# Performance work log

Hardware: AMD Instinct MI355X
Metric: run time of the kernel (lower is better)

Reference implementation:

```python
import jax, jax.numpy as jnp
import numpy as np

B, N, T, F = 64, 1024, 64, 8
IN = T * F      # LSTMCell input size = 512
H = T           # LSTMCell hidden size = 64


def setup_inputs() -> dict:
    key = jax.random.key(0)
    k1, k2, k3, k4, k5 = jax.random.split(key, 5)
    s_ih = 1.0 / np.sqrt(H)
    return {
        "x": jax.random.normal(k1, (B, N, T, F), dtype=jnp.float32),
        "W_ih": jax.random.uniform(k2, (4 * H, IN), minval=-s_ih, maxval=s_ih, dtype=jnp.float32),
        "W_hh": jax.random.uniform(k3, (4 * H, H), minval=-s_ih, maxval=s_ih, dtype=jnp.float32),
        "b_ih": jax.random.uniform(k4, (4 * H,), minval=-s_ih, maxval=s_ih, dtype=jnp.float32),
        "b_hh": jax.random.uniform(k5, (4 * H,), minval=-s_ih, maxval=s_ih, dtype=jnp.float32),
    }


def _lstm_scan(x_seq, W_ih, W_hh, b_ih, b_hh):
    # x_seq: (n, b, t*f). Recurrent scan over the node dimension.
    b = x_seq.shape[1]
    h0 = jnp.zeros((b, H), dtype=x_seq.dtype)
    c0 = jnp.zeros((b, H), dtype=x_seq.dtype)
    # Precompute input projections for all steps at once (big GEMM).
    xg = jnp.einsum('nbi,gi->nbg', x_seq, W_ih) + b_ih + b_hh  # (n, b, 4H)

    def step(carry, xg_t):
        h, c = carry
        gates = xg_t + h @ W_hh.T                # (b, 4H)
        i, f, g, o = jnp.split(gates, 4, axis=-1)
        i = jax.nn.sigmoid(i)
        f = jax.nn.sigmoid(f)
        g = jnp.tanh(g)
        o = jax.nn.sigmoid(o)
        c_new = f * c + i * g
        h_new = o * jnp.tanh(c_new)
        return (h_new, c_new), h_new

    _, hs = jax.lax.scan(step, (h0, c0), xg)     # hs: (n, b, H)
    return hs


def reference(x, W_ih, W_hh, b_ih, b_hh):
    b, n, t, f = x.shape
    x_em = x.reshape(b, n, t * f).transpose(1, 0, 2)   # (n, b, t*f)
    hs = _lstm_scan(x_em, W_ih, W_hh, b_ih, b_hh)      # (n, b, t)
    return hs.transpose(1, 0, 2)                        # (b, n, t)
```

## Files before the change

### kernel.cpp

```cpp
#include <hip/hip_runtime.h>
#include <math.h>

#define B_  64
#define N_  1024
#define H_  64
#define IN_ 512
#define G4  256

__global__ __launch_bounds__(256) void gemm_xg_kernel(
    const float* __restrict__ x,
    const float* __restrict__ Wih,
    const float* __restrict__ bih,
    const float* __restrict__ bhh,
    float* __restrict__ xg)
{
    __shared__ float As[32][68];
    __shared__ float Bs[32][68];

    const int tid = threadIdx.x;
    const int g0  = blockIdx.x * 64;
    const int m0  = blockIdx.y * 64;

    const int tx = tid & 15;
    const int ty = tid >> 4;

    const int arow = tid >> 3;
    const int ak4  = tid & 7;
    const int brow = tid >> 2;
    const int bk4  = tid & 3;

    float acc[4][4] = {{0.f}};

    for (int k0 = 0; k0 < IN_; k0 += 32) {
        #pragma unroll
        for (int half = 0; half < 2; ++half) {
            const int ml = arow + half * 32;
            const int m  = m0 + ml;
            const int bb = m & 63;
            const int nn = m >> 6;
            const float4 v = *(const float4*)&x[((size_t)(bb * N_ + nn)) * IN_ + k0 + ak4 * 4];
            As[ak4 * 4 + 0][ml] = v.x;
            As[ak4 * 4 + 1][ml] = v.y;
            As[ak4 * 4 + 2][ml] = v.z;
            As[ak4 * 4 + 3][ml] = v.w;
        }
        #pragma unroll
        for (int half = 0; half < 2; ++half) {
            const int kq = bk4 + half * 4;
            const float4 v = *(const float4*)&Wih[(size_t)(g0 + brow) * IN_ + k0 + kq * 4];
            Bs[kq * 4 + 0][brow] = v.x;
            Bs[kq * 4 + 1][brow] = v.y;
            Bs[kq * 4 + 2][brow] = v.z;
            Bs[kq * 4 + 3][brow] = v.w;
        }
        __syncthreads();

        #pragma unroll
        for (int k = 0; k < 32; ++k) {
            const float4 av = *(const float4*)&As[k][ty * 4];
            const float4 bv = *(const float4*)&Bs[k][tx * 4];
            const float ar[4] = {av.x, av.y, av.z, av.w};
            const float br[4] = {bv.x, bv.y, bv.z, bv.w};
            #pragma unroll
            for (int i = 0; i < 4; ++i)
                #pragma unroll
                for (int j = 0; j < 4; ++j)
                    acc[i][j] = fmaf(ar[i], br[j], acc[i][j]);
        }
        __syncthreads();
    }

    float bias[4];
    #pragma unroll
    for (int j = 0; j < 4; ++j)
        bias[j] = bih[g0 + tx * 4 + j] + bhh[g0 + tx * 4 + j];

    #pragma unroll
    for (int i = 0; i < 4; ++i) {
        const int m = m0 + ty * 4 + i;
        float4 o;
        o.x = acc[i][0] + bias[0];
        o.y = acc[i][1] + bias[1];
        o.z = acc[i][2] + bias[2];
        o.w = acc[i][3] + bias[3];
        *(float4*)&xg[(size_t)m * G4 + g0 + tx * 4] = o;
    }
}

__device__ __forceinline__ float fast_rcp(float x) {
    return __builtin_amdgcn_rcpf(x);
}

template <int CTRL>
__device__ __forceinline__ float dppf(float x) {
    return __int_as_float(__builtin_amdgcn_mov_dpp(
        __float_as_int(x), CTRL, 0xF, 0xF, true));
}
#define DPP_QSWAP1 0xB1
#define DPP_SHR4   0x114
#define DPP_SHR2   0x112

__global__ __launch_bounds__(512) void lstm_scan_kernel(
    const float* __restrict__ xg,
    const float* __restrict__ Whh,
    float* __restrict__ out)
{
    const int t    = threadIdx.x;
    const int bb   = blockIdx.x;
    const int w    = t >> 6;
    const int ln   = t & 63;
    const int half = ln & 1;
    const int gidx = (ln >> 1) & 3;
    const int cell = (w << 3) | (ln >> 3);
    const int grow = (gidx << 6) | cell;

    __shared__ float h_sh[2][64];

    float4 w4[8];
    {
        const float* wrow = &Whh[(size_t)grow * H_ + half * 32];
        #pragma unroll
        for (int q = 0; q < 8; ++q)
            w4[q] = *(const float4*)&wrow[q * 4];
    }
    #pragma unroll
    for (int q = 0; q < 8; ++q)
        asm volatile("" : "+v"(w4[q].x), "+v"(w4[q].y), "+v"(w4[q].z), "+v"(w4[q].w));

    const float Ac = (gidx == 2) ? 1.f : 0.f;
    const float Bc = (gidx == 2) ? -2.f : 1.f;
    const float Cc = (gidx == 2) ? 2.f : -1.f;
    const bool  is_o = (gidx == 3);
    const bool  is_writer = ((ln & 7) == 6);
    const bool  carries_xg = (half == 0);

    float c = 0.f;
    if (t < 64) h_sh[0][t] = 0.f;
    __syncthreads();

    int cur = 0;
    const size_t xg_base = (size_t)bb * G4 + grow;
    const size_t xg_nstride = (size_t)B_ * G4;

    float p0 = xg[xg_base + 0 * xg_nstride];
    float p1 = xg[xg_base + 1 * xg_nstride];
    float p2 = xg[xg_base + 2 * xg_nstride];
    float p3 = xg[xg_base + 3 * xg_nstride];

    auto step = [&](int n, float xg_cur) {
        const float* hb = &h_sh[cur][half * 32];
        float b0 = carries_xg ? xg_cur : 0.f;
        float b1 = 0.f, b2 = 0.f, b3 = 0.f;
        float b4 = 0.f, b5 = 0.f, b6 = 0.f, b7 = 0.f;
        #pragma unroll
        for (int q = 0; q < 8; q += 2) {
            const float4 h0 = *(const float4*)&hb[q * 4];
            const float4 h1 = *(const float4*)&hb[q * 4 + 4];
            b0 = fmaf(w4[q].x,     h0.x, b0);
            b1 = fmaf(w4[q].y,     h0.y, b1);
            b2 = fmaf(w4[q].z,     h0.z, b2);
            b3 = fmaf(w4[q].w,     h0.w, b3);
            b4 = fmaf(w4[q + 1].x, h1.x, b4);
            b5 = fmaf(w4[q + 1].y, h1.y, b5);
            b6 = fmaf(w4[q + 1].z, h1.z, b6);
            b7 = fmaf(w4[q + 1].w, h1.w, b7);
        }
        float acc = ((b0 + b4) + (b1 + b5)) + ((b2 + b6) + (b3 + b7));
        acc += dppf<DPP_QSWAP1>(acc);

        const float v = fmaf(Bc, fast_rcp(1.f + __expf(Cc * acc)), Ac);

        const float u  = is_o ? c : v;
        const float t_ = dppf<DPP_SHR4>(u);
        const float w_ = u * t_;
        const float s  = w_ + dppf<DPP_SHR2>(w_);
        const float th = fmaf(-2.f, fast_rcp(1.f + __expf(2.f * s)), 1.f);
        const float h  = v * th;
        c = s;

        if (is_writer) {
            h_sh[cur ^ 1][cell] = h;
            out[((size_t)bb * N_ + n) * H_ + cell] = h;
        }

        asm volatile("s_waitcnt lgkmcnt(0)" ::: "memory");
        __builtin_amdgcn_s_barrier();
        asm volatile("" ::: "memory");

        cur ^= 1;
    };

    for (int n = 0; n < N_; n += 4) {
        step(n + 0, p0);
        p0 = xg[xg_base + (size_t)((n + 4 < N_) ? n + 4 : N_ - 1) * xg_nstride];
        step(n + 1, p1);
        p1 = xg[xg_base + (size_t)((n + 5 < N_) ? n + 5 : N_ - 1) * xg_nstride];
        step(n + 2, p2);
        p2 = xg[xg_base + (size_t)((n + 6 < N_) ? n + 6 : N_ - 1) * xg_nstride];
        step(n + 3, p3);
        p3 = xg[xg_base + (size_t)((n + 7 < N_) ? n + 7 : N_ - 1) * xg_nstride];
    }
}

extern "C" void kernel_launch(void* const* d_in, const int* in_sizes, int n_in,
                              void* d_out, int out_size, void* d_ws, size_t ws_size,
                              hipStream_t stream)
{
    const float* x   = (const float*)d_in[0];
    const float* Wih = (const float*)d_in[1];
    const float* Whh = (const float*)d_in[2];
    const float* bih = (const float*)d_in[3];
    const float* bhh = (const float*)d_in[4];
    float* out = (float*)d_out;
    float* xg  = (float*)d_ws;

    dim3 ggrid(4, 1024);
    gemm_xg_kernel<<<ggrid, 256, 0, stream>>>(x, Wih, bih, bhh, xg);
    lstm_scan_kernel<<<64, 512, 0, stream>>>(xg, Whh, out);
}
```

Baseline: 707.5 us.

## Assign one full gate row per lane and halve scan block to four waves

The scan kernel now gives each lane a complete 64-wide W_hh row, held as 16 float4 registers in a rotated order. The four gates of a cell sit in a lane quad, and h values are rotated across the quad with DPP so each lane reads only a quarter of h from LDS. This drops the cross-lane partial-sum reduction and cuts the block from 512 to 256 threads, so each per-step barrier synchronises fewer waves. The cost is more VGPRs per lane (64 for weights) and a longer serial FMA chain per lane.

```diff
diff --git a/kernel.cpp b/kernel.cpp
--- a/kernel.cpp
+++ b/kernel.cpp
@@ -96,11 +96,20 @@
     return __int_as_float(__builtin_amdgcn_mov_dpp(
         __float_as_int(x), CTRL, 0xF, 0xF, true));
 }
-#define DPP_QSWAP1 0xB1
-#define DPP_SHR4   0x114
-#define DPP_SHR2   0x112
-
-__global__ __launch_bounds__(512) void lstm_scan_kernel(
+#define DPP_ROT1   0x39
+#define DPP_G_T    0x44
+#define DPP_G_S    0x90
+
+__device__ __forceinline__ float4 qrot1(float4 v) {
+    float4 r;
+    r.x = dppf<DPP_ROT1>(v.x);
+    r.y = dppf<DPP_ROT1>(v.y);
+    r.z = dppf<DPP_ROT1>(v.z);
+    r.w = dppf<DPP_ROT1>(v.w);
+    return r;
+}
+
+__global__ __launch_bounds__(256, 1) void lstm_scan_kernel(
     const float* __restrict__ xg,
     const float* __restrict__ Whh,
     float* __restrict__ out)
@@ -109,30 +118,29 @@
     const int bb   = blockIdx.x;
     const int w    = t >> 6;
     const int ln   = t & 63;
-    const int half = ln & 1;
-    const int gidx = (ln >> 1) & 3;
-    const int cell = (w << 3) | (ln >> 3);
-    const int grow = (gidx << 6) | cell;
+    const int qpos = ln & 3;
+    const int cell = (w << 4) | (ln >> 2);
+    const int grow = (qpos << 6) | cell;
 
     __shared__ float h_sh[2][64];
 
-    float4 w4[8];
+    float4 wst[16];
     {
-        const float* wrow = &Whh[(size_t)grow * H_ + half * 32];
-        #pragma unroll
-        for (int q = 0; q < 8; ++q)
-            w4[q] = *(const float4*)&wrow[q * 4];
+        const float* wrow = &Whh[(size_t)grow * H_];
+        #pragma unroll
+        for (int r = 0; r < 4; ++r)
+            #pragma unroll
+            for (int s = 0; s < 4; ++s)
+                wst[r * 4 + s] = *(const float4*)&wrow[(4 * r + ((qpos + s) & 3)) * 4];
     }
     #pragma unroll
-    for (int q = 0; q < 8; ++q)
-        asm volatile("" : "+v"(w4[q].x), "+v"(w4[q].y), "+v"(w4[q].z), "+v"(w4[q].w));
-
-    const float Ac = (gidx == 2) ? 1.f : 0.f;
-    const float Bc = (gidx == 2) ? -2.f : 1.f;
-    const float Cc = (gidx == 2) ? 2.f : -1.f;
-    const bool  is_o = (gidx == 3);
-    const bool  is_writer = ((ln & 7) == 6);
-    const bool  carries_xg = (half == 0);
+    for (int q = 0; q < 16; ++q)
+        asm volatile("" : "+v"(wst[q].x), "+v"(wst[q].y), "+v"(wst[q].z), "+v"(wst[q].w));
+
+    const float Ac = (qpos == 2) ? 1.f : 0.f;
+    const float Bc = (qpos == 2) ? -2.f : 1.f;
+    const float Cc = (qpos == 2) ? 2.f : -1.f;
+    const bool  is_o = (qpos == 3);
 
     float c = 0.f;
     if (t < 64) h_sh[0][t] = 0.f;
@@ -148,37 +156,76 @@
     float p3 = xg[xg_base + 3 * xg_nstride];
 
     auto step = [&](int n, float xg_cur) {
-        const float* hb = &h_sh[cur][half * 32];
-        float b0 = carries_xg ? xg_cur : 0.f;
-        float b1 = 0.f, b2 = 0.f, b3 = 0.f;
-        float b4 = 0.f, b5 = 0.f, b6 = 0.f, b7 = 0.f;
-        #pragma unroll
-        for (int q = 0; q < 8; q += 2) {
-            const float4 h0 = *(const float4*)&hb[q * 4];
-            const float4 h1 = *(const float4*)&hb[q * 4 + 4];
-            b0 = fmaf(w4[q].x,     h0.x, b0);
-            b1 = fmaf(w4[q].y,     h0.y, b1);
-            b2 = fmaf(w4[q].z,     h0.z, b2);
-            b3 = fmaf(w4[q].w,     h0.w, b3);
-            b4 = fmaf(w4[q + 1].x, h1.x, b4);
-            b5 = fmaf(w4[q + 1].y, h1.y, b5);
-            b6 = fmaf(w4[q + 1].z, h1.z, b6);
-            b7 = fmaf(w4[q + 1].w, h1.w, b7);
-        }
-        float acc = ((b0 + b4) + (b1 + b5)) + ((b2 + b6) + (b3 + b7));
-        acc += dppf<DPP_QSWAP1>(acc);
+        const float* hb = h_sh[cur];
+        float4 h0 = *(const float4*)&hb[(0  + qpos) * 4];
+        float4 h1 = *(const float4*)&hb[(4  + qpos) * 4];
+        float4 h2 = *(const float4*)&hb[(8  + qpos) * 4];
+        float4 h3 = *(const float4*)&hb[(12 + qpos) * 4];
+
+        float b0 = xg_cur, b1 = 0.f, b2 = 0.f, b3 = 0.f;
+        float b4 = 0.f,    b5 = 0.f, b6 = 0.f, b7 = 0.f;
+
+        b0 = fmaf(wst[0].x, h0.x, b0); b1 = fmaf(wst[0].y, h0.y, b1);
+        b2 = fmaf(wst[0].z, h0.z, b2); b3 = fmaf(wst[0].w, h0.w, b3);
+        h0 = qrot1(h0);
+        b4 = fmaf(wst[1].x, h0.x, b4); b5 = fmaf(wst[1].y, h0.y, b5);
+        b6 = fmaf(wst[1].z, h0.z, b6); b7 = fmaf(wst[1].w, h0.w, b7);
+        h0 = qrot1(h0);
+        b0 = fmaf(wst[2].x, h0.x, b0); b1 = fmaf(wst[2].y, h0.y, b1);
+        b2 = fmaf(wst[2].z, h0.z, b2); b3 = fmaf(wst[2].w, h0.w, b3);
+        h0 = qrot1(h0);
+        b4 = fmaf(wst[3].x, h0.x, b4); b5 = fmaf(wst[3].y, h0.y, b5);
+        b6 = fmaf(wst[3].z, h0.z, b6); b7 = fmaf(wst[3].w, h0.w, b7);
+
+        b0 = fmaf(wst[4].x, h1.x, b0); b1 = fmaf(wst[4].y, h1.y, b1);
+        b2 = fmaf(wst[4].z, h1.z, b2); b3 = fmaf(wst[4].w, h1.w, b3);
+        h1 = qrot1(h1);
+        b4 = fmaf(wst[5].x, h1.x, b4); b5 = fmaf(wst[5].y, h1.y, b5);
+        b6 = fmaf(wst[5].z, h1.z, b6); b7 = fmaf(wst[5].w, h1.w, b7);
+        h1 = qrot1(h1);
+        b0 = fmaf(wst[6].x, h1.x, b0); b1 = fmaf(wst[6].y, h1.y, b1);
+        b2 = fmaf(wst[6].z, h1.z, b2); b3 = fmaf(wst[6].w, h1.w, b3);
+        h1 = qrot1(h1);
+        b4 = fmaf(wst[7].x, h1.x, b4); b5 = fmaf(wst[7].y, h1.y, b5);
+        b6 = fmaf(wst[7].z, h1.z, b6); b7 = fmaf(wst[7].w, h1.w, b7);
+
+        b0 = fmaf(wst[8].x, h2.x, b0); b1 = fmaf(wst[8].y, h2.y, b1);
+        b2 = fmaf(wst[8].z, h2.z, b2); b3 = fmaf(wst[8].w, h2.w, b3);
+        h2 = qrot1(h2);
+        b4 = fmaf(wst[9].x, h2.x, b4); b5 = fmaf(wst[9].y, h2.y, b5);
+        b6 = fmaf(wst[9].z, h2.z, b6); b7 = fmaf(wst[9].w, h2.w, b7);
+        h2 = qrot1(h2);
+        b0 = fmaf(wst[10].x, h2.x, b0); b1 = fmaf(wst[10].y, h2.y, b1);
+        b2 = fmaf(wst[10].z, h2.z, b2); b3 = fmaf(wst[10].w, h2.w, b3);
+        h2 = qrot1(h2);
+        b4 = fmaf(wst[11].x, h2.x, b4); b5 = fmaf(wst[11].y, h2.y, b5);
+        b6 = fmaf(wst[11].z, h2.z, b6); b7 = fmaf(wst[11].w, h2.w, b7);
+
+        b0 = fmaf(wst[12].x, h3.x, b0); b1 = fmaf(wst[12].y, h3.y, b1);
+        b2 = fmaf(wst[12].z, h3.z, b2); b3 = fmaf(wst[12].w, h3.w, b3);
+        h3 = qrot1(h3);
+        b4 = fmaf(wst[13].x, h3.x, b4); b5 = fmaf(wst[13].y, h3.y, b5);
+        b6 = fmaf(wst[13].z, h3.z, b6); b7 = fmaf(wst[13].w, h3.w, b7);
+        h3 = qrot1(h3);
+        b0 = fmaf(wst[14].x, h3.x, b0); b1 = fmaf(wst[14].y, h3.y, b1);
+        b2 = fmaf(wst[14].z, h3.z, b2); b3 = fmaf(wst[14].w, h3.w, b3);
+        h3 = qrot1(h3);
+        b4 = fmaf(wst[15].x, h3.x, b4); b5 = fmaf(wst[15].y, h3.y, b5);
+        b6 = fmaf(wst[15].z, h3.z, b6); b7 = fmaf(wst[15].w, h3.w, b7);
+
+        const float acc = ((b0 + b4) + (b1 + b5)) + ((b2 + b6) + (b3 + b7));
 
         const float v = fmaf(Bc, fast_rcp(1.f + __expf(Cc * acc)), Ac);
 
         const float u  = is_o ? c : v;
-        const float t_ = dppf<DPP_SHR4>(u);
+        const float t_ = dppf<DPP_G_T>(u);
         const float w_ = u * t_;
-        const float s  = w_ + dppf<DPP_SHR2>(w_);
-        const float th = fmaf(-2.f, fast_rcp(1.f + __expf(2.f * s)), 1.f);
+        const float s_ = w_ + dppf<DPP_G_S>(w_);
+        const float th = fmaf(-2.f, fast_rcp(1.f + __expf(2.f * s_)), 1.f);
         const float h  = v * th;
-        c = s;
-
-        if (is_writer) {
+        c = s_;
+
+        if (is_o) {
             h_sh[cur ^ 1][cell] = h;
             out[((size_t)bb * N_ + n) * H_ + cell] = h;
         }
@@ -216,5 +263,5 @@
 
     dim3 ggrid(4, 1024);
     gemm_xg_kernel<<<ggrid, 256, 0, stream>>>(x, Wih, bih, bhh, xg);
-    lstm_scan_kernel<<<64, 512, 0, stream>>>(xg, Whh, out);
-}
+    lstm_scan_kernel<<<64, 256, 0, stream>>>(xg, Whh, out);
+}
```

New measurement: 771.9 us. +9.1%, slower.

## Rewrite input-projection GEMM with bf16 MFMA and register prefetch

Applied to the files above, without the earlier changes.

Replaces the fp32 SIMT tiled GEMM for the input projection with a bf16 MFMA kernel that uses 128x128 tiles, 512 threads and register double-buffering of the next K slice. Inputs are rounded to bf16 when stored to shared memory, and accumulation stays in fp32. The goal is to cut GEMM compute time, which is a large share of the total next to the sequential scan. The cost is reduced precision in xg, which could push the results past the tolerance.

```diff
diff --git a/kernel.cpp b/kernel.cpp
--- a/kernel.cpp
+++ b/kernel.cpp
@@ -7,83 +7,118 @@
 #define IN_ 512
 #define G4  256
 
-__global__ __launch_bounds__(256) void gemm_xg_kernel(
+typedef __attribute__((ext_vector_type(8))) short bf16x8;
+typedef __attribute__((ext_vector_type(4))) float f32x4;
+
+__device__ __forceinline__ unsigned short f2bf(float f) {
+    unsigned u = __float_as_uint(f);
+    u += 0x7FFFu + ((u >> 16) & 1u);
+    return (unsigned short)(u >> 16);
+}
+
+__device__ __forceinline__ bf16x8 pack8(const float4 a, const float4 b) {
+    bf16x8 r;
+    r[0] = (short)f2bf(a.x); r[1] = (short)f2bf(a.y);
+    r[2] = (short)f2bf(a.z); r[3] = (short)f2bf(a.w);
+    r[4] = (short)f2bf(b.x); r[5] = (short)f2bf(b.y);
+    r[6] = (short)f2bf(b.z); r[7] = (short)f2bf(b.w);
+    return r;
+}
+
+#define PADK 72
+
+__global__ __launch_bounds__(512) void gemm_xg_mfma(
     const float* __restrict__ x,
     const float* __restrict__ Wih,
     const float* __restrict__ bih,
     const float* __restrict__ bhh,
     float* __restrict__ xg)
 {
-    __shared__ float As[32][68];
-    __shared__ float Bs[32][68];
-
-    const int tid = threadIdx.x;
-    const int g0  = blockIdx.x * 64;
-    const int m0  = blockIdx.y * 64;
-
-    const int tx = tid & 15;
-    const int ty = tid >> 4;
-
-    const int arow = tid >> 3;
-    const int ak4  = tid & 7;
-    const int brow = tid >> 2;
-    const int bk4  = tid & 3;
-
-    float acc[4][4] = {{0.f}};
-
-    for (int k0 = 0; k0 < IN_; k0 += 32) {
-        #pragma unroll
-        for (int half = 0; half < 2; ++half) {
-            const int ml = arow + half * 32;
-            const int m  = m0 + ml;
-            const int bb = m & 63;
-            const int nn = m >> 6;
-            const float4 v = *(const float4*)&x[((size_t)(bb * N_ + nn)) * IN_ + k0 + ak4 * 4];
-            As[ak4 * 4 + 0][ml] = v.x;
-            As[ak4 * 4 + 1][ml] = v.y;
-            As[ak4 * 4 + 2][ml] = v.z;
-            As[ak4 * 4 + 3][ml] = v.w;
-        }
-        #pragma unroll
-        for (int half = 0; half < 2; ++half) {
-            const int kq = bk4 + half * 4;
-            const float4 v = *(const float4*)&Wih[(size_t)(g0 + brow) * IN_ + k0 + kq * 4];
-            Bs[kq * 4 + 0][brow] = v.x;
-            Bs[kq * 4 + 1][brow] = v.y;
-            Bs[kq * 4 + 2][brow] = v.z;
-            Bs[kq * 4 + 3][brow] = v.w;
-        }
+    __shared__ unsigned short As[128 * PADK];
+    __shared__ unsigned short Bs[128 * PADK];
+
+    const int tid  = threadIdx.x;
+    const int n0   = blockIdx.x * 128;
+    const int m0   = blockIdx.y * 128;
+
+    const int lane = tid & 63;
+    const int wid  = tid >> 6;
+    const int wr   = wid & 3;
+    const int wc   = wid >> 2;
+
+    const int srow = tid >> 2;
+    const int sk   = (tid & 3) * 16;
+
+    const int mrow = m0 + srow;
+    const float* ag = &x[((size_t)((mrow & 63) * N_ + (mrow >> 6))) * IN_];
+    const float* bg = &Wih[(size_t)(n0 + srow) * IN_];
+
+    f32x4 acc[2][4];
+    #pragma unroll
+    for (int i = 0; i < 2; ++i)
+        #pragma unroll
+        for (int j = 0; j < 4; ++j)
+            acc[i][j] = (f32x4){0.f, 0.f, 0.f, 0.f};
+
+    float4 a0 = *(const float4*)&ag[sk + 0];
+    float4 a1 = *(const float4*)&ag[sk + 4];
+    float4 a2 = *(const float4*)&ag[sk + 8];
+    float4 a3 = *(const float4*)&ag[sk + 12];
+    float4 b0 = *(const float4*)&bg[sk + 0];
+    float4 b1 = *(const float4*)&bg[sk + 4];
+    float4 b2 = *(const float4*)&bg[sk + 8];
+    float4 b3 = *(const float4*)&bg[sk + 12];
+
+    for (int k0 = 0; k0 < IN_; k0 += 64) {
+        *(bf16x8*)&As[srow * PADK + sk + 0] = pack8(a0, a1);
+        *(bf16x8*)&As[srow * PADK + sk + 8] = pack8(a2, a3);
+        *(bf16x8*)&Bs[srow * PADK + sk + 0] = pack8(b0, b1);
+        *(bf16x8*)&Bs[srow * PADK + sk + 8] = pack8(b2, b3);
         __syncthreads();
 
-        #pragma unroll
-        for (int k = 0; k < 32; ++k) {
-            const float4 av = *(const float4*)&As[k][ty * 4];
-            const float4 bv = *(const float4*)&Bs[k][tx * 4];
-            const float ar[4] = {av.x, av.y, av.z, av.w};
-            const float br[4] = {bv.x, bv.y, bv.z, bv.w};
-            #pragma unroll
-            for (int i = 0; i < 4; ++i)
+        if (k0 + 64 < IN_) {
+            const int kn = k0 + 64;
+            a0 = *(const float4*)&ag[kn + sk + 0];
+            a1 = *(const float4*)&ag[kn + sk + 4];
+            a2 = *(const float4*)&ag[kn + sk + 8];
+            a3 = *(const float4*)&ag[kn + sk + 12];
+            b0 = *(const float4*)&bg[kn + sk + 0];
+            b1 = *(const float4*)&bg[kn + sk + 4];
+            b2 = *(const float4*)&bg[kn + sk + 8];
+            b3 = *(const float4*)&bg[kn + sk + 12];
+        }
+
+        #pragma unroll
+        for (int kk = 0; kk < 2; ++kk) {
+            const int kof = kk * 32 + (lane >> 4) * 8;
+            bf16x8 af[2], bfr[4];
+            #pragma unroll
+            for (int i = 0; i < 2; ++i)
+                af[i] = *(const bf16x8*)&As[(wr * 32 + i * 16 + (lane & 15)) * PADK + kof];
+            #pragma unroll
+            for (int j = 0; j < 4; ++j)
+                bfr[j] = *(const bf16x8*)&Bs[(wc * 64 + j * 16 + (lane & 15)) * PADK + kof];
+            #pragma unroll
+            for (int i = 0; i < 2; ++i)
                 #pragma unroll
                 for (int j = 0; j < 4; ++j)
-                    acc[i][j] = fmaf(ar[i], br[j], acc[i][j]);
+                    acc[i][j] = __builtin_amdgcn_mfma_f32_16x16x32_bf16(
+                        af[i], bfr[j], acc[i][j], 0, 0, 0);
         }
         __syncthreads();
     }
 
-    float bias[4];
     #pragma unroll
-    for (int j = 0; j < 4; ++j)
-        bias[j] = bih[g0 + tx * 4 + j] + bhh[g0 + tx * 4 + j];
-
-    #pragma unroll
-    for (int i = 0; i < 4; ++i) {
-        const int m = m0 + ty * 4 + i;
-        float4 o;
-        o.x = acc[i][0] + bias[0];
-        o.y = acc[i][1] + bias[1];
-        o.z = acc[i][2] + bias[2];
-        o.w = acc[i][3] + bias[3];
-        *(float4*)&xg[(size_t)m * G4 + g0 + tx * 4] = o;
+    for (int j = 0; j < 4; ++j) {
+        const int col = n0 + wc * 64 + j * 16 + (lane & 15);
+        const float bias = bih[col] + bhh[col];
+        #pragma unroll
+        for (int i = 0; i < 2; ++i) {
+            const int rbase = m0 + wr * 32 + i * 16 + (lane >> 4) * 4;
+            #pragma unroll
+            for (int r = 0; r < 4; ++r)
+                xg[(size_t)(rbase + r) * G4 + col] = acc[i][j][r] + bias;
+        }
     }
 }
 
@@ -214,7 +249,7 @@
     float* out = (float*)d_out;
     float* xg  = (float*)d_ws;
 
-    dim3 ggrid(4, 1024);
-    gemm_xg_kernel<<<ggrid, 256, 0, stream>>>(x, Wih, bih, bhh, xg);
+    dim3 ggrid(2, 512);
+    gemm_xg_mfma<<<ggrid, 512, 0, stream>>>(x, Wih, bih, bhh, xg);
     lstm_scan_kernel<<<64, 512, 0, stream>>>(xg, Whh, out);
 }
```

New measurement: 583.9 us. 17.5% less time.
